# Optimization experiments

Hardware: AMD Instinct MI355X
Metric: run time of the kernel (lower is better)

The kernel has to match this reference:

```python
import jax, jax.numpy as jnp
import numpy as np

N = 50000
E = 800000
IN_DIM = 128
HID = 64
HEADS = 4
OUT_DIM = 64
NEG_SLOPE = 0.2


def setup_inputs() -> dict:
    key = jax.random.key(0)
    ks = jax.random.split(key, 10)
    x = jax.random.normal(ks[0], (N, IN_DIM), dtype=jnp.float32)
    edge_index = jax.random.randint(ks[1], (2, E), 0, N, dtype=jnp.int64)
    s1 = 1.0 / np.sqrt(IN_DIM)
    s2 = 1.0 / np.sqrt(HEADS * HID)
    return {
        "x": x,
        "edge_index": edge_index,
        "W1": jax.random.normal(ks[2], (IN_DIM, HEADS * HID), dtype=jnp.float32) * s1,
        "a_src1": jax.random.normal(ks[3], (HEADS, HID), dtype=jnp.float32) * s2,
        "a_dst1": jax.random.normal(ks[4], (HEADS, HID), dtype=jnp.float32) * s2,
        "b1": jnp.zeros((HEADS * HID,), dtype=jnp.float32),
        "W2": jax.random.normal(ks[5], (HEADS * HID, OUT_DIM), dtype=jnp.float32) * s2,
        "a_src2": jax.random.normal(ks[6], (1, OUT_DIM), dtype=jnp.float32) * 0.125,
        "a_dst2": jax.random.normal(ks[7], (1, OUT_DIM), dtype=jnp.float32) * 0.125,
        "b2": jnp.zeros((OUT_DIM,), dtype=jnp.float32),
    }


def gat_layer(x, src, dst, W, a_src, a_dst, bias, heads, ch, concat):
    n = x.shape[0]
    h = (x @ W).reshape(n, heads, ch)                      # [N,H,C]
    asrc = jnp.einsum('nhc,hc->nh', h, a_src)              # [N,H]
    adst = jnp.einsum('nhc,hc->nh', h, a_dst)              # [N,H]
    e = asrc[src] + adst[dst]                              # [E',H]
    e = jnp.where(e > 0, e, NEG_SLOPE * e)                 # LeakyReLU(0.2)
    # segment softmax over incoming edges of each dst node
    m = jax.ops.segment_max(e, dst, num_segments=n)        # [N,H]
    m = jnp.where(jnp.isfinite(m), m, 0.0)
    ex = jnp.exp(e - m[dst])
    denom = jax.ops.segment_sum(ex, dst, num_segments=n)   # [N,H]
    alpha = ex / (denom[dst] + 1e-16)                      # [E',H]
    out = jax.ops.segment_sum(alpha[:, :, None] * h[src], dst, num_segments=n)  # [N,H,C]
    if concat:
        out = out.reshape(n, heads * ch)
    else:
        out = out.mean(axis=1)
    return out + bias


def reference(x, edge_index, W1, a_src1, a_dst1, b1, W2, a_src2, a_dst2, b2):
    n = x.shape[0]
    loops = jnp.arange(n, dtype=edge_index.dtype)
    src = jnp.concatenate([edge_index[0], loops])          # add self-loops (PyG default)
    dst = jnp.concatenate([edge_index[1], loops])
    h = gat_layer(x, src, dst, W1, a_src1, a_dst1, b1, HEADS, HID, True)
    h = jax.nn.elu(h)
    out = gat_layer(h, src, dst, W2, a_src2, a_dst2, b2, 1, OUT_DIM, False)
    return out
```

## Files before the change

kernel.cpp:

```cpp
#include <hip/hip_runtime.h>
#include <hip/hip_bf16.h>

#define NN 50000
#define EE 800000
#define IN_DIM 128
#define HH 256
#define HID 64
#define HEADS 4
#define OUT_DIM 64
#define SCAN_BLOCKS 196

static __device__ __forceinline__ unsigned short f2bf(float f) {
    unsigned int u = __float_as_uint(f);
    u += 0x7fffu + ((u >> 16) & 1u);
    return (unsigned short)(u >> 16);
}
static __device__ __forceinline__ float bf2f(unsigned short h) {
    return __uint_as_float(((unsigned int)h) << 16);
}


__global__ void hist_kernel(const int* __restrict__ ei, int* __restrict__ deg) {
    int e = blockIdx.x * 256 + threadIdx.x;
    atomicAdd(&deg[ei[EE + e]], 1);
}

__global__ __launch_bounds__(256) void block_scan_kernel(
    const int* __restrict__ deg, int* __restrict__ local_scan,
    int* __restrict__ block_sum) {
    __shared__ int tmp[256];
    int t = threadIdx.x, i = blockIdx.x * 256 + t;
    int v = (i < NN) ? deg[i] : 0;
    tmp[t] = v;
    __syncthreads();
    for (int d = 1; d < 256; d <<= 1) {
        int u = (t >= d) ? tmp[t - d] : 0;
        __syncthreads();
        tmp[t] += u;
        __syncthreads();
    }
    if (i < NN) local_scan[i] = tmp[t] - v;
    if (t == 255) block_sum[blockIdx.x] = tmp[255];
}

__global__ __launch_bounds__(256) void scan_sums_kernel(int* __restrict__ block_sum) {
    __shared__ int tmp[256];
    int t = threadIdx.x;
    int v = (t < SCAN_BLOCKS) ? block_sum[t] : 0;
    tmp[t] = v;
    __syncthreads();
    for (int d = 1; d < 256; d <<= 1) {
        int u = (t >= d) ? tmp[t - d] : 0;
        __syncthreads();
        tmp[t] += u;
        __syncthreads();
    }
    if (t < SCAN_BLOCKS) block_sum[t] = tmp[t] - v;
}

__global__ __launch_bounds__(256) void finalize_kernel(
    const int* __restrict__ local_scan, const int* __restrict__ block_sum,
    int* __restrict__ row_ptr, int* __restrict__ cursor) {
    int i = blockIdx.x * 256 + threadIdx.x;
    if (i < NN) {
        int v = local_scan[i] + block_sum[blockIdx.x];
        row_ptr[i] = v; cursor[i] = v;
    }
    if (i == 0) row_ptr[NN] = EE;
}

__global__ void scatter_kernel(const int* __restrict__ ei, int* __restrict__ cursor,
                               int* __restrict__ edge_src) {
    int e = blockIdx.x * 256 + threadIdx.x;
    int d = ei[EE + e];
    int pos = atomicAdd(&cursor[d], 1);
    edge_src[pos] = ei[e];
}


__global__ __launch_bounds__(256) void gemm1_kernel(
    const float* __restrict__ x, const float* __restrict__ W1,
    const float* __restrict__ a_src1, const float* __restrict__ a_dst1,
    unsigned short* __restrict__ h1, float* __restrict__ asrc1, float* __restrict__ adst1) {
    __shared__ __align__(16) float xs[16][IN_DIM];
    int t = threadIdx.x;
    int row0 = blockIdx.x * 16;
    #pragma unroll
    for (int j = 0; j < 8; j++) {
        int idx = t + j * 256;
        int r = idx >> 7, k = idx & 127;
        xs[r][k] = x[(size_t)(row0 + r) * IN_DIM + k];
    }
    __syncthreads();
    float acc[16];
    #pragma unroll
    for (int r = 0; r < 16; r++) acc[r] = 0.f;
    for (int k = 0; k < IN_DIM; k += 4) {
        float w0 = W1[(k + 0) * HH + t];
        float w1 = W1[(k + 1) * HH + t];
        float w2 = W1[(k + 2) * HH + t];
        float w3 = W1[(k + 3) * HH + t];
        #pragma unroll
        for (int r = 0; r < 16; r++) {
            float4 xv = *reinterpret_cast<const float4*>(&xs[r][k]);
            acc[r] = fmaf(xv.x, w0, acc[r]);
            acc[r] = fmaf(xv.y, w1, acc[r]);
            acc[r] = fmaf(xv.z, w2, acc[r]);
            acc[r] = fmaf(xv.w, w3, acc[r]);
        }
    }
    #pragma unroll
    for (int r = 0; r < 16; r++)
        h1[(size_t)(row0 + r) * HH + t] = f2bf(acc[r]);
    float as = a_src1[t];
    float ad = a_dst1[t];
    int lane = t & 63, head = t >> 6;
    #pragma unroll
    for (int r = 0; r < 16; r++) {
        float vs = acc[r] * as, vd = acc[r] * ad;
        #pragma unroll
        for (int o = 32; o > 0; o >>= 1) { vs += __shfl_xor(vs, o); vd += __shfl_xor(vd, o); }
        if (lane == 0) {
            asrc1[(row0 + r) * HEADS + head] = vs;
            adst1[(row0 + r) * HEADS + head] = vd;
        }
    }
}


__global__ __launch_bounds__(256) void agg1_kernel(
    const int* __restrict__ row_ptr, const int* __restrict__ edge_src,
    const unsigned short* __restrict__ h1, const float* __restrict__ asrc1,
    const float* __restrict__ adst1, const float* __restrict__ b1,
    float* __restrict__ x2) {
    int wid = threadIdx.x >> 6, lane = threadIdx.x & 63;
    int node = blockIdx.x * 4 + wid;
    int head = lane >> 4;
    float ad = adst1[node * HEADS + head];
    int beg = row_ptr[node], end = row_ptr[node + 1];
    float denom = 0.f;
    float ax = 0.f, ay = 0.f, az = 0.f, aw = 0.f;
    int sA = (beg < end) ? edge_src[beg] : node;
    int sB = (beg + 1 < end) ? edge_src[beg + 1] : node;
    float eA = asrc1[sA * HEADS + head];
    float eB = asrc1[sB * HEADS + head];
    ushort4 hA = *reinterpret_cast<const ushort4*>(&h1[(size_t)sA * HH + lane * 4]);
    ushort4 hB = *reinterpret_cast<const ushort4*>(&h1[(size_t)sB * HH + lane * 4]);
    for (int i = beg; i <= end; i++) {
        int j = i + 2;
        int sC = (j < end) ? edge_src[j] : node;
        float eC = asrc1[sC * HEADS + head];
        ushort4 hC = *reinterpret_cast<const ushort4*>(&h1[(size_t)sC * HH + lane * 4]);
        float e = eA + ad;
        e = e > 0.f ? e : 0.2f * e;
        float ex = __expf(e);
        denom += ex;
        ax = fmaf(ex, bf2f(hA.x), ax); ay = fmaf(ex, bf2f(hA.y), ay);
        az = fmaf(ex, bf2f(hA.z), az); aw = fmaf(ex, bf2f(hA.w), aw);
        eA = eB; hA = hB;
        eB = eC; hB = hC;
    }
    float inv = 1.0f / (denom + 1e-16f);
    int cb = lane * 4;
    float v0 = ax * inv + b1[cb + 0];
    float v1 = ay * inv + b1[cb + 1];
    float v2 = az * inv + b1[cb + 2];
    float v3 = aw * inv + b1[cb + 3];
    v0 = v0 > 0.f ? v0 : (__expf(v0) - 1.f);
    v1 = v1 > 0.f ? v1 : (__expf(v1) - 1.f);
    v2 = v2 > 0.f ? v2 : (__expf(v2) - 1.f);
    v3 = v3 > 0.f ? v3 : (__expf(v3) - 1.f);
    float4 o; o.x = v0; o.y = v1; o.z = v2; o.w = v3;
    *reinterpret_cast<float4*>(&x2[(size_t)node * HH + cb]) = o;
}


__global__ __launch_bounds__(256) void gemm2_kernel(
    const float* __restrict__ x2, const float* __restrict__ W2,
    const float* __restrict__ a_src2, const float* __restrict__ a_dst2,
    unsigned short* __restrict__ h2, float* __restrict__ asrc2, float* __restrict__ adst2) {
    __shared__ __align__(16) float xs[16][HH];
    int t = threadIdx.x;
    int row0 = blockIdx.x * 16;
    #pragma unroll
    for (int j = 0; j < 16; j++) {
        int idx = t + j * 256;
        int r = idx >> 8, k = idx & 255;
        xs[r][k] = x2[(size_t)(row0 + r) * HH + k];
    }
    __syncthreads();
    int c = t & 63, rg = t >> 6;
    float acc[4] = {0.f, 0.f, 0.f, 0.f};
    for (int k = 0; k < HH; k += 4) {
        float w0 = W2[(k + 0) * OUT_DIM + c];
        float w1 = W2[(k + 1) * OUT_DIM + c];
        float w2 = W2[(k + 2) * OUT_DIM + c];
        float w3 = W2[(k + 3) * OUT_DIM + c];
        #pragma unroll
        for (int i = 0; i < 4; i++) {
            int r = rg + i * 4;
            float4 xv = *reinterpret_cast<const float4*>(&xs[r][k]);
            acc[i] = fmaf(xv.x, w0, acc[i]);
            acc[i] = fmaf(xv.y, w1, acc[i]);
            acc[i] = fmaf(xv.z, w2, acc[i]);
            acc[i] = fmaf(xv.w, w3, acc[i]);
        }
    }
    float as = a_src2[c], ad = a_dst2[c];
    #pragma unroll
    for (int i = 0; i < 4; i++) {
        int row = row0 + rg + i * 4;
        h2[(size_t)row * OUT_DIM + c] = f2bf(acc[i]);
        float vs = acc[i] * as, vd = acc[i] * ad;
        #pragma unroll
        for (int o = 32; o > 0; o >>= 1) { vs += __shfl_xor(vs, o); vd += __shfl_xor(vd, o); }
        if (c == 0) { asrc2[row] = vs; adst2[row] = vd; }
    }
}


__global__ __launch_bounds__(256) void agg2_kernel(
    const int* __restrict__ row_ptr, const int* __restrict__ edge_src,
    const unsigned short* __restrict__ h2, const float* __restrict__ asrc2,
    const float* __restrict__ adst2, const float* __restrict__ b2,
    float* __restrict__ out) {
    int wid = threadIdx.x >> 6, lane = threadIdx.x & 63;
    int node = blockIdx.x * 4 + wid;
    float ad = adst2[node];
    int beg = row_ptr[node], end = row_ptr[node + 1];
    float denom = 0.f, acc = 0.f;
    int sA = (beg < end) ? edge_src[beg] : node;
    int sB = (beg + 1 < end) ? edge_src[beg + 1] : node;
    float eA = asrc2[sA], eB = asrc2[sB];
    unsigned short hA = h2[(size_t)sA * OUT_DIM + lane];
    unsigned short hB = h2[(size_t)sB * OUT_DIM + lane];
    for (int i = beg; i <= end; i++) {
        int j = i + 2;
        int sC = (j < end) ? edge_src[j] : node;
        float eC = asrc2[sC];
        unsigned short hC = h2[(size_t)sC * OUT_DIM + lane];
        float e = eA + ad;
        e = e > 0.f ? e : 0.2f * e;
        float ex = __expf(e);
        denom += ex;
        acc = fmaf(ex, bf2f(hA), acc);
        eA = eB; hA = hB;
        eB = eC; hB = hC;
    }
    out[(size_t)node * OUT_DIM + lane] = acc / (denom + 1e-16f) + b2[lane];
}


extern "C" void kernel_launch(void* const* d_in, const int* in_sizes, int n_in,
                              void* d_out, int out_size, void* d_ws, size_t ws_size,
                              hipStream_t stream) {
    const float* x   = (const float*)d_in[0];
    const int*   ei  = (const int*)d_in[1];
    const float* W1  = (const float*)d_in[2];
    const float* as1 = (const float*)d_in[3];
    const float* ad1 = (const float*)d_in[4];
    const float* b1  = (const float*)d_in[5];
    const float* W2  = (const float*)d_in[6];
    const float* as2 = (const float*)d_in[7];
    const float* ad2 = (const float*)d_in[8];
    const float* b2  = (const float*)d_in[9];
    float* out = (float*)d_out;

    char* ws = (char*)d_ws;
    size_t off = 0;
    auto alloc = [&](size_t bytes) -> void* {
        void* p = ws + off;
        off += (bytes + 255) & ~(size_t)255;
        return p;
    };
    unsigned short* h1 = (unsigned short*)alloc((size_t)NN * HH * 2);
    float* x2     = (float*)alloc((size_t)NN * HH * 4);
    unsigned short* h2 = (unsigned short*)alloc((size_t)NN * OUT_DIM * 2);
    float* asrc1  = (float*)alloc((size_t)NN * HEADS * 4);
    float* adst1  = (float*)alloc((size_t)NN * HEADS * 4);
    float* asrc2  = (float*)alloc((size_t)NN * 4);
    float* adst2  = (float*)alloc((size_t)NN * 4);
    int*   deg    = (int*)alloc((size_t)NN * 4);
    int*   row_ptr= (int*)alloc((size_t)(NN + 1) * 4);
    int*   cursor = (int*)alloc((size_t)NN * 4);
    int*   edge_src=(int*)alloc((size_t)EE * 4);
    int*   local_scan = (int*)alloc((size_t)NN * 4);
    int*   block_sum  = (int*)alloc((size_t)SCAN_BLOCKS * 4);

    hipMemsetAsync(deg, 0, (size_t)NN * 4, stream);
    hist_kernel<<<EE / 256, 256, 0, stream>>>(ei, deg);
    block_scan_kernel<<<SCAN_BLOCKS, 256, 0, stream>>>(deg, local_scan, block_sum);
    scan_sums_kernel<<<1, 256, 0, stream>>>(block_sum);
    finalize_kernel<<<SCAN_BLOCKS, 256, 0, stream>>>(local_scan, block_sum, row_ptr, cursor);
    scatter_kernel<<<EE / 256, 256, 0, stream>>>(ei, cursor, edge_src);

    gemm1_kernel<<<NN / 16, 256, 0, stream>>>(x, W1, as1, ad1, h1, asrc1, adst1);
    agg1_kernel<<<NN / 4, 256, 0, stream>>>(row_ptr, edge_src, h1, asrc1, adst1, b1, x2);
    gemm2_kernel<<<NN / 16, 256, 0, stream>>>(x2, W2, as2, ad2, h2, asrc2, adst2);
    agg2_kernel<<<NN / 4, 256, 0, stream>>>(row_ptr, edge_src, h2, asrc2, adst2, b2, out);
}
```

Measured before the change: 425.3 us.

## Register-tile gemm1 with 16x4 outputs per thread and vectorize tile loads

gemm1 now processes 64 rows per block, and each thread computes a 16-row by 4-column register tile. Weights are read as float4, so each W1 element fetched from global memory is reused across more rows, and shared-memory x reads are reused across 4 columns. The attention-score reduction shrinks to a 16-lane shuffle per head, and bf16 stores become ushort4. The x tile loads in both GEMMs switch to float4, and row clamping plus guards handle the partial last block. The cost is higher register pressure from 64 float accumulators, which may lower occupancy.

Measured after the change: 398.7 us. 1.07x faster.

```diff
diff --git a/kernel.cpp b/kernel.cpp
--- a/kernel.cpp
+++ b/kernel.cpp
@@ -82,47 +82,61 @@
     const float* __restrict__ x, const float* __restrict__ W1,
     const float* __restrict__ a_src1, const float* __restrict__ a_dst1,
     unsigned short* __restrict__ h1, float* __restrict__ asrc1, float* __restrict__ adst1) {
-    __shared__ __align__(16) float xs[16][IN_DIM];
+    __shared__ __align__(16) float xs[64][IN_DIM];
     int t = threadIdx.x;
-    int row0 = blockIdx.x * 16;
+    int row0 = blockIdx.x * 64;
     #pragma unroll
     for (int j = 0; j < 8; j++) {
         int idx = t + j * 256;
-        int r = idx >> 7, k = idx & 127;
-        xs[r][k] = x[(size_t)(row0 + r) * IN_DIM + k];
+        int r = idx >> 5, k4 = (idx & 31) * 4;
+        int rr = row0 + r; if (rr >= NN) rr = NN - 1;
+        *reinterpret_cast<float4*>(&xs[r][k4]) =
+            *reinterpret_cast<const float4*>(&x[(size_t)rr * IN_DIM + k4]);
     }
     __syncthreads();
-    float acc[16];
-    #pragma unroll
-    for (int r = 0; r < 16; r++) acc[r] = 0.f;
+    int lane = t & 63, wid = t >> 6;
+    float4 acc[16];
+    #pragma unroll
+    for (int r = 0; r < 16; r++) acc[r] = make_float4(0.f, 0.f, 0.f, 0.f);
+    const float* wbase = W1 + lane * 4;
     for (int k = 0; k < IN_DIM; k += 4) {
-        float w0 = W1[(k + 0) * HH + t];
-        float w1 = W1[(k + 1) * HH + t];
-        float w2 = W1[(k + 2) * HH + t];
-        float w3 = W1[(k + 3) * HH + t];
+        float4 w0 = *reinterpret_cast<const float4*>(&wbase[(k + 0) * HH]);
+        float4 w1 = *reinterpret_cast<const float4*>(&wbase[(k + 1) * HH]);
+        float4 w2 = *reinterpret_cast<const float4*>(&wbase[(k + 2) * HH]);
+        float4 w3 = *reinterpret_cast<const float4*>(&wbase[(k + 3) * HH]);
         #pragma unroll
         for (int r = 0; r < 16; r++) {
-            float4 xv = *reinterpret_cast<const float4*>(&xs[r][k]);
-            acc[r] = fmaf(xv.x, w0, acc[r]);
-            acc[r] = fmaf(xv.y, w1, acc[r]);
-            acc[r] = fmaf(xv.z, w2, acc[r]);
-            acc[r] = fmaf(xv.w, w3, acc[r]);
+            float4 xv = *reinterpret_cast<const float4*>(&xs[wid * 16 + r][k]);
+            acc[r].x = fmaf(xv.x, w0.x, acc[r].x); acc[r].y = fmaf(xv.x, w0.y, acc[r].y);
+            acc[r].z = fmaf(xv.x, w0.z, acc[r].z); acc[r].w = fmaf(xv.x, w0.w, acc[r].w);
+            acc[r].x = fmaf(xv.y, w1.x, acc[r].x); acc[r].y = fmaf(xv.y, w1.y, acc[r].y);
+            acc[r].z = fmaf(xv.y, w1.z, acc[r].z); acc[r].w = fmaf(xv.y, w1.w, acc[r].w);
+            acc[r].x = fmaf(xv.z, w2.x, acc[r].x); acc[r].y = fmaf(xv.z, w2.y, acc[r].y);
+            acc[r].z = fmaf(xv.z, w2.z, acc[r].z); acc[r].w = fmaf(xv.z, w2.w, acc[r].w);
+            acc[r].x = fmaf(xv.w, w3.x, acc[r].x); acc[r].y = fmaf(xv.w, w3.y, acc[r].y);
+            acc[r].z = fmaf(xv.w, w3.z, acc[r].z); acc[r].w = fmaf(xv.w, w3.w, acc[r].w);
         }
     }
-    #pragma unroll
-    for (int r = 0; r < 16; r++)
-        h1[(size_t)(row0 + r) * HH + t] = f2bf(acc[r]);
-    float as = a_src1[t];
-    float ad = a_dst1[t];
-    int lane = t & 63, head = t >> 6;
+    float4 asv = *reinterpret_cast<const float4*>(&a_src1[lane * 4]);
+    float4 adv = *reinterpret_cast<const float4*>(&a_dst1[lane * 4]);
+    int head = lane >> 4;
     #pragma unroll
     for (int r = 0; r < 16; r++) {
-        float vs = acc[r] * as, vd = acc[r] * ad;
+        int row = row0 + wid * 16 + r;
+        bool ok = row < NN;
+        if (ok) {
+            ushort4 hv;
+            hv.x = f2bf(acc[r].x); hv.y = f2bf(acc[r].y);
+            hv.z = f2bf(acc[r].z); hv.w = f2bf(acc[r].w);
+            *reinterpret_cast<ushort4*>(&h1[(size_t)row * HH + lane * 4]) = hv;
+        }
+        float vs = acc[r].x * asv.x + acc[r].y * asv.y + acc[r].z * asv.z + acc[r].w * asv.w;
+        float vd = acc[r].x * adv.x + acc[r].y * adv.y + acc[r].z * adv.z + acc[r].w * adv.w;
         #pragma unroll
-        for (int o = 32; o > 0; o >>= 1) { vs += __shfl_xor(vs, o); vd += __shfl_xor(vd, o); }
-        if (lane == 0) {
-            asrc1[(row0 + r) * HEADS + head] = vs;
-            adst1[(row0 + r) * HEADS + head] = vd;
+        for (int o = 1; o < 16; o <<= 1) { vs += __shfl_xor(vs, o); vd += __shfl_xor(vd, o); }
+        if (ok && (lane & 15) == 0) {
+            asrc1[row * HEADS + head] = vs;
+            adst1[row * HEADS + head] = vd;
         }
     }
 }
@@ -183,10 +197,11 @@
     int t = threadIdx.x;
     int row0 = blockIdx.x * 16;
     #pragma unroll
-    for (int j = 0; j < 16; j++) {
+    for (int j = 0; j < 4; j++) {
         int idx = t + j * 256;
-        int r = idx >> 8, k = idx & 255;
-        xs[r][k] = x2[(size_t)(row0 + r) * HH + k];
+        int r = idx >> 6, k4 = (idx & 63) * 4;
+        *reinterpret_cast<float4*>(&xs[r][k4]) =
+            *reinterpret_cast<const float4*>(&x2[(size_t)(row0 + r) * HH + k4]);
     }
     __syncthreads();
     int c = t & 63, rg = t >> 6;
@@ -294,7 +309,7 @@
     finalize_kernel<<<SCAN_BLOCKS, 256, 0, stream>>>(local_scan, block_sum, row_ptr, cursor);
     scatter_kernel<<<EE / 256, 256, 0, stream>>>(ei, cursor, edge_src);
 
-    gemm1_kernel<<<NN / 16, 256, 0, stream>>>(x, W1, as1, ad1, h1, asrc1, adst1);
+    gemm1_kernel<<<(NN + 63) / 64, 256, 0, stream>>>(x, W1, as1, ad1, h1, asrc1, adst1);
     agg1_kernel<<<NN / 4, 256, 0, stream>>>(row_ptr, edge_src, h1, asrc1, adst1, b1, x2);
     gemm2_kernel<<<NN / 16, 256, 0, stream>>>(x2, W2, as2, ad2, h2, asrc2, adst2);
     agg2_kernel<<<NN / 4, 256, 0, stream>>>(row_ptr, edge_src, h2, asrc2, adst2, b2, out);
```
